# Optimization experiments

Measured on AMD Instinct MI355X. Metric: run time of the kernel, lower is better.

Reference implementation:

```python
import jax, jax.numpy as jnp
import numpy as np

N_NODES = 20000
N_EDGES = 400000
DIM = 128       # dim
NB = 16         # radial basis size
ZD = 16         # species encoding dim
N_SPECIES = 51
CUTOFF = 5.0
NLAYERS = 2
N_ONSITE = 3


def radial_basis(r):
    # 'gaussian_rinv': gaussians placed uniformly in inverse-distance space (HIP-NN style)
    rinv = 1.0 / r
    mus = jnp.linspace(1.0 / CUTOFF, 1.0, NB, dtype=r.dtype)
    sigma = mus[1] - mus[0]
    return jnp.exp(-0.5 * ((rinv[:, None] - mus[None, :]) / sigma) ** 2)  # [E, NB]


def setup_inputs() -> dict:
    key = jax.random.key(0)
    ks = jax.random.split(key, 16)
    species = jax.random.randint(ks[0], (N_NODES,), 1, N_SPECIES)
    edge_src = jax.random.randint(ks[1], (N_EDGES,), 0, N_NODES)
    edge_dst = jax.random.randint(ks[2], (N_EDGES,), 0, N_NODES)
    distances = jax.random.uniform(ks[3], (N_EDGES,), minval=0.8, maxval=CUTOFF)
    switch = jax.random.uniform(ks[4], (N_EDGES,))
    Z = jax.random.normal(ks[5], (N_SPECIES, ZD))  # species encoding table
    Ws0 = jax.random.normal(ks[6], (ZD, DIM)) / np.sqrt(ZD)
    bs0 = jnp.zeros((DIM,), jnp.float32)
    V0 = jax.random.normal(ks[7], (NB, ZD, DIM)) / np.sqrt(NB * ZD)
    Ws1 = jax.random.normal(ks[8], (DIM, DIM)) / np.sqrt(DIM)
    bs1 = jnp.zeros((DIM,), jnp.float32)
    V1 = jax.random.normal(ks[9], (NB, DIM, DIM)) / np.sqrt(NB * DIM)
    Won_a = jax.random.normal(ks[10], (NLAYERS, N_ONSITE, DIM, DIM)) / np.sqrt(DIM)
    bon_a = jnp.zeros((NLAYERS, N_ONSITE, DIM), jnp.float32)
    Won_b = jax.random.normal(ks[11], (NLAYERS, N_ONSITE, DIM, DIM)) / np.sqrt(DIM)
    bon_b = jnp.zeros((NLAYERS, N_ONSITE, DIM), jnp.float32)
    return dict(species=species, edge_src=edge_src, edge_dst=edge_dst,
                distances=distances, switch=switch, Z=Z,
                Ws0=Ws0, bs0=bs0, V0=V0, Ws1=Ws1, bs1=bs1, V1=V1,
                Won_a=Won_a, bon_a=bon_a, Won_b=Won_b, bon_b=bon_b)


def reference(species, edge_src, edge_dst, distances, switch, Z,
              Ws0, bs0, V0, Ws1, bs1, V1, Won_a, bon_a, Won_b, bon_b):
    zi = Z[species]                       # [N, ZD] species encoding
    s = radial_basis(distances)           # [E, NB] (identical basis each layer)
    sw = switch[:, None]                  # [E, 1]
    Ws, bs, Vs = (Ws0, Ws1), (bs0, bs1), (V0, V1)
    zis = []
    for layer in range(NLAYERS):
        zself = zi @ Ws[layer] + bs[layer]                        # [N, DIM]
        # mij = einsum('ej,ek,jkl->el', s, zi[edge_dst], V): per-edge outer then one GEMM
        zdst = zi[edge_dst]                                       # [E, k] gather
        outer = s[:, :, None] * zdst[:, None, :]                  # [E, NB, k]
        mij = outer.reshape(outer.shape[0], -1) @ Vs[layer].reshape(-1, DIM)  # [E, DIM]
        zi = jax.nn.silu(zself.at[edge_src].add(mij * sw))        # scatter-add
        for j in range(N_ONSITE):                                 # residual 2-layer MLPs
            h = jax.nn.silu(zi @ Won_a[layer, j] + bon_a[layer, j])
            zi = zi + h @ Won_b[layer, j] + bon_b[layer, j]
        zis.append(zi)
    # (embedding, embedding_layers)
    return zi, jnp.stack(zis, axis=1)
```

## Files before the change

kernel.cpp:

```cpp
#include <hip/hip_runtime.h>
#include <stdint.h>

#define NNODES 20000
#define NEDGES 400000
#define MTILES 1250
#define MT2    625
#define KS1 68

typedef __attribute__((ext_vector_type(8))) short short8;
typedef __attribute__((ext_vector_type(4))) float floatx4;

__device__ __forceinline__ float bf2f(uint16_t u){ return __uint_as_float(((uint32_t)u)<<16); }
__device__ __forceinline__ uint16_t f2bf(float f){
  uint32_t x = __float_as_uint(f);
  x += 0x7FFFu + ((x>>16)&1u);
  return (uint16_t)(x>>16);
}
__device__ __forceinline__ uint32_t packbf(float a, float b){
  return (uint32_t)f2bf(a) | ((uint32_t)f2bf(b)<<16);
}
__device__ __forceinline__ float siluf(float x){ return x/(1.0f+__expf(-x)); }
__device__ __forceinline__ float ldf(const void* p, int i, int md){
  return (md==1) ? bf2f(((const uint16_t*)p)[i]) : ((const float*)p)[i];
}

#define OFF_V0   0
#define N_V0     32768
#define OFF_WS1  32768
#define N_WS1    16384
#define OFF_BS1  49152
#define N_BS1    128
#define OFF_V1   49280
#define N_V1     262144
#define OFF_WA   311424
#define N_WA     98304
#define OFF_BA   409728
#define N_BA     768
#define OFF_WB   410496
#define N_WB     98304
#define OFF_BB   508800
#define N_BB     768
#define N_CONV   509568

__global__ void k_probe(const void* dist, int* mode){
  if(threadIdx.x != 0 || blockIdx.x != 0) return;
  const float* f = (const float*)dist;
  const uint16_t* h = (const uint16_t*)dist;
  int okf = 1, okb = 1;
  for(int i=0;i<256;i++){
    float a = f[i];       okf &= (a >= 0.7f) & (a <= 5.1f);
    float b = bf2f(h[i]); okb &= (b >= 0.7f) & (b <= 5.1f);
  }
  *mode = okb ? 1 : (okf ? 0 : 1);
}

__global__ __launch_bounds__(256) void k_conv(const void* s0,const void* s1,const void* s2,const void* s3,
                                              const void* s4,const void* s5,const void* s6,const void* s7,
                                              const int* __restrict__ modep, float* __restrict__ dst){
  int md = *modep;
  int i = blockIdx.x*256 + threadIdx.x;
  if(i >= N_CONV) return;
  const void* src; int t = i;
  if(t < N_V0){src=s0;}
  else if((t-=N_V0) < N_WS1){src=s1;}
  else if((t-=N_WS1) < N_BS1){src=s2;}
  else if((t-=N_BS1) < N_V1){src=s3;}
  else if((t-=N_V1) < N_WA){src=s4;}
  else if((t-=N_WA) < N_BA){src=s5;}
  else if((t-=N_BA) < N_WB){src=s6;}
  else {t-=N_WB; src=s7;}
  dst[i] = ldf(src, t, md);
}

__global__ __launch_bounds__(256) void k_hist(const int* __restrict__ src, int* __restrict__ cnt){
  int e = blockIdx.x*256 + threadIdx.x;
  if(e < NEDGES){
    int s = src[e];
    if((unsigned)s < NNODES) atomicAdd(&cnt[s], 1);
  }
}

__global__ __launch_bounds__(1024) void k_scan(int* cnt_cur, int* offs){
  __shared__ int wsum[16];
  int t = threadIdx.x;
  const int chunk = (NNODES + 1023)/1024;
  int lo = t*chunk, hi = lo+chunk;
  if(lo > NNODES) lo = NNODES;
  if(hi > NNODES) hi = NNODES;
  int s = 0;
  for(int i=lo;i<hi;i++) s += cnt_cur[i];
  int lane = t&63, wv = t>>6;
  int v = s;
  #pragma unroll
  for(int d=1; d<64; d<<=1){
    int u = __shfl_up(v, d);
    if(lane >= d) v += u;
  }
  if(lane==63) wsum[wv] = v;
  __syncthreads();
  if(t==0){
    int run = 0;
    #pragma unroll
    for(int i=0;i<16;i++){ int c = wsum[i]; wsum[i] = run; run += c; }
  }
  __syncthreads();
  int run = wsum[wv] + (v - s);
  for(int i=lo;i<hi;i++){
    int c = cnt_cur[i];
    offs[i] = run;
    cnt_cur[i] = run;
    run += c;
  }
  if(t==1023) offs[NNODES] = run;
}

__global__ __launch_bounds__(256) void k_fill(const int* __restrict__ src,
                                              const int* __restrict__ edst,
                                              const int* __restrict__ species,
                                              int* __restrict__ cur,
                                              int* __restrict__ dsts,
                                              int* __restrict__ sps,
                                              int* __restrict__ pos){
  int e = blockIdx.x*256 + threadIdx.x;
  if(e >= NEDGES) return;
  int s = src[e];
  if((unsigned)s >= NNODES) s = 0;
  int p = atomicAdd(&cur[s], 1);
  if((unsigned)p >= NEDGES) p = 0;
  pos[e] = p;
  int dn = edst[e];
  if((unsigned)dn >= NNODES) dn = 0;
  dsts[p] = dn;
  int sp = species[dn];
  if((unsigned)sp >= 51) sp = 0;
  sps[p] = sp;
}

__global__ __launch_bounds__(256) void k_G(const void* __restrict__ dist,
                                           const void* __restrict__ sw,
                                           const int* __restrict__ modep,
                                           const int* __restrict__ pos,
                                           uint16_t* __restrict__ gs){
  int e = blockIdx.x*256 + threadIdx.x;
  if(e >= NEDGES) return;
  int md = *modep;
  float r = ldf(dist, e, md);
  float w = ldf(sw, e, md);
  float rinv = 1.0f/r;
  const float sigma = 0.8f/15.0f;
  const float isig  = 15.0f/0.8f;
  uint32_t u[8];
  #pragma unroll
  for(int j=0;j<8;j++){
    float mu0 = 0.2f + sigma*(float)(2*j);
    float mu1 = 0.2f + sigma*(float)(2*j+1);
    float t0 = (rinv-mu0)*isig, t1 = (rinv-mu1)*isig;
    u[j] = packbf(w*__expf(-0.5f*t0*t0), w*__expf(-0.5f*t1*t1));
  }
  int p = pos[e];
  uint4* o = (uint4*)(gs + (size_t)p*16);
  o[0] = make_uint4(u[0],u[1],u[2],u[3]);
  o[1] = make_uint4(u[4],u[5],u[6],u[7]);
}

__global__ __launch_bounds__(128) void k_spec(const void* __restrict__ Z,
                                              const void* __restrict__ Ws0,
                                              const void* __restrict__ bs0,
                                              const int* __restrict__ modep,
                                              float* __restrict__ ZWs0,
                                              uint16_t* __restrict__ zfb){
  int s = blockIdx.x, d = threadIdx.x;
  int md = *modep;
  float zk[16];
  #pragma unroll
  for(int k=0;k<16;k++) zk[k] = ldf(Z, s*16+k, md);
  float a = ldf(bs0, d, md);
  #pragma unroll
  for(int k=0;k<16;k++) a = fmaf(zk[k], ldf(Ws0, k*128+d, md), a);
  ZWs0[s*128+d] = a;
  if(d < 16) zfb[s*16+d] = f2bf(zk[d]);
}

__global__ __launch_bounds__(256) void k_prepB(const float* __restrict__ W, int Ksteps,
                                               uint16_t* __restrict__ Bf){
  int idx = blockIdx.x*256 + threadIdx.x;
  int total = Ksteps*8*64;
  if(idx >= total) return;
  int l = idx & 63, nt = (idx>>6)&7, kk = idx>>9;
  int kbase = kk*32 + (l>>4)*8;
  int dim = nt*16 + (l&15);
  uint32_t u[4];
  #pragma unroll
  for(int t=0;t<4;t++){
    float f0 = W[(size_t)(kbase+2*t)*128 + dim];
    float f1 = W[(size_t)(kbase+2*t+1)*128 + dim];
    u[t] = packbf(f0,f1);
  }
  ((uint4*)Bf)[idx] = make_uint4(u[0],u[1],u[2],u[3]);
}

__global__ __launch_bounds__(256) void k_prepW(const float* __restrict__ conv,
                                               uint16_t* __restrict__ Wf){
  int idx = blockIdx.x*256 + threadIdx.x;
  if(idx >= 12*2048) return;
  int wi = idx>>11, r = idx&2047;
  int l = r & 63, nt = (r>>6)&7, kk = r>>9;
  const float* W = conv + ((wi<6) ? (OFF_WA + wi*16384) : (OFF_WB + (wi-6)*16384));
  int kbase = kk*32 + (l>>4)*8;
  int dim = nt*16 + (l&15);
  uint32_t u[4];
  #pragma unroll
  for(int t=0;t<4;t++){
    float f0 = W[(size_t)(kbase+2*t)*128 + dim];
    float f1 = W[(size_t)(kbase+2*t+1)*128 + dim];
    u[t] = packbf(f0,f1);
  }
  ((uint4*)Wf)[idx] = make_uint4(u[0],u[1],u[2],u[3]);
}

__global__ __launch_bounds__(256) void k_msg0f(const int* __restrict__ offs,
                                               const int* __restrict__ sps,
                                               const uint16_t* __restrict__ gs,
                                               const uint16_t* __restrict__ zfb,
                                               const uint16_t* __restrict__ Bf,
                                               const int* __restrict__ species,
                                               const float* __restrict__ ZWs0,
                                               float* __restrict__ zi){
  __shared__ uint16_t ldsA[8*64*8];
  int w = threadIdx.x>>6, l = threadIdx.x&63;
  int n0 = blockIdx.x*16;
  int col = l&15, quad = l>>4;
  for(int i=0;i<4;i++){
    int m = w*4 + i;
    int n = n0 + m;
    int beg = offs[n], end = offs[n+1];
    floatx4 acc0 = (floatx4){0.f,0.f,0.f,0.f};
    for(int p0=beg; p0<end; p0+=32){
      int sp[8];
      union { short8 s; uint16_t u[8]; } Bg, Az;
      #pragma unroll
      for(int j=0;j<8;j++){
        int p = p0 + quad*8 + j;
        int pc = p < end ? p : beg;
        sp[j] = sps[pc];
        uint16_t g = gs[(size_t)pc*16 + col];
        Bg.u[j] = (p < end) ? g : (uint16_t)0;
      }
      #pragma unroll
      for(int j=0;j<8;j++)
        Az.u[j] = zfb[sp[j]*16 + col];
      acc0 = __builtin_amdgcn_mfma_f32_16x16x32_bf16(Az.s, Bg.s, acc0, 0,0,0);
    }
    int K0 = col*16 + quad*4;
    int kk = K0>>5, qt = (K0>>3)&3, jt = K0&7;
    int slot = kk*64 + ((qt*16 + m) ^ (kk>>2));
    uint32_t lo = packbf(acc0[0], acc0[1]);
    uint32_t hi = packbf(acc0[2], acc0[3]);
    *(uint2*)(&ldsA[slot*8 + jt]) = make_uint2(lo, hi);
  }
  __syncthreads();
  floatx4 acc1 = (floatx4){0.f,0.f,0.f,0.f};
  floatx4 acc2 = (floatx4){0.f,0.f,0.f,0.f};
  const short8* Bp = (const short8*)Bf;
  int nt1 = w, nt2 = w+4;
  #pragma unroll
  for(int kk=0;kk<8;kk++){
    short8 a = *(const short8*)(&ldsA[(kk*64 + (l^(kk>>2)))*8]);
    short8 b1 = Bp[(size_t)(kk*8+nt1)*64 + l];
    short8 b2 = Bp[(size_t)(kk*8+nt2)*64 + l];
    acc1 = __builtin_amdgcn_mfma_f32_16x16x32_bf16(a, b1, acc1, 0,0,0);
    acc2 = __builtin_amdgcn_mfma_f32_16x16x32_bf16(a, b2, acc2, 0,0,0);
  }
  #pragma unroll
  for(int reg=0;reg<4;reg++){
    int node = n0 + quad*4 + reg;
    int sp = species[node];
    if((unsigned)sp >= 51) sp = 0;
    int d1 = nt1*16 + col, d2 = nt2*16 + col;
    zi[(size_t)node*128 + d1] = siluf(acc1[reg] + ZWs0[sp*128 + d1]);
    zi[(size_t)node*128 + d2] = siluf(acc2[reg] + ZWs0[sp*128 + d2]);
  }
}

__global__ __launch_bounds__(1024, 2) void k_msg1f(const int* __restrict__ offs,
                                               const int* __restrict__ dsts,
                                               const uint16_t* __restrict__ gs,
                                               const uint16_t* __restrict__ zib,
                                               const uint16_t* __restrict__ zib2,
                                               const uint16_t* __restrict__ Bf,
                                               const float* __restrict__ bias,
                                               float* __restrict__ zacc){
  __shared__ __align__(16) uint16_t ldsA[2*64*64*8];
  int w = threadIdx.x>>6, l = threadIdx.x&63;
  int n0 = blockIdx.x*32;
  int col = l&15, quad = l>>4;
  for(int i=0;i<2;i++){
    int m = w*2 + i;
    int n = n0 + m;
    int beg = offs[n], end = offs[n+1];
    floatx4 acc[8];
    #pragma unroll
    for(int t=0;t<8;t++) acc[t] = (floatx4){0.f,0.f,0.f,0.f};
    for(int p0=beg; p0<end; p0+=32){
      int dn[8];
      union { short8 s; uint16_t u[8]; } Bg;
      #pragma unroll
      for(int j=0;j<8;j++){
        int p = p0 + quad*8 + j;
        int pc = p < end ? p : beg;
        dn[j] = dsts[pc];
        uint16_t g = gs[(size_t)pc*16 + col];
        Bg.u[j] = (p < end) ? g : (uint16_t)0;
      }
      uint4 row[8];
      #pragma unroll
      for(int j=0;j<8;j++)
        row[j] = *(const uint4*)(zib2 + (size_t)dn[j]*128 + col*8);
      #pragma unroll
      for(int mt=0;mt<8;mt++){
        union { short8 s; uint32_t u32[4]; } Az;
        #pragma unroll
        for(int cp=0;cp<4;cp++){
          uint32_t a = ((const uint32_t*)&row[2*cp])[mt>>1];
          uint32_t b = ((const uint32_t*)&row[2*cp+1])[mt>>1];
          Az.u32[cp] = __builtin_amdgcn_perm(b, a, (mt&1) ? 0x07060302u : 0x05040100u);
        }
        acc[mt] = __builtin_amdgcn_mfma_f32_16x16x32_bf16(Az.s, Bg.s, acc[mt], 0,0,0);
      }
    }
    uint16_t* tile = ldsA + (size_t)(m>>4)*32768;
    int mloc = m & 15;
    #pragma unroll
    for(int mt=0;mt<8;mt++){
      int K0 = col*128 + mt*16 + quad*4;
      int kk = K0>>5, qt = (K0>>3)&3, jt = K0&7;
      int slot = kk*64 + ((qt*16 + mloc) ^ (kk>>2));
      uint32_t lo = packbf(acc[mt][0], acc[mt][1]);
      uint32_t hi = packbf(acc[mt][2], acc[mt][3]);
      *(uint2*)(&tile[slot*8 + jt]) = make_uint2(lo, hi);
    }
  }
  __syncthreads();
  int nt1 = w & 7, half = w >> 3;
  floatx4 accA = (floatx4){0.f,0.f,0.f,0.f};
  floatx4 accB = (floatx4){0.f,0.f,0.f,0.f};
  const short8* Bp = (const short8*)Bf;
  int kb = half*32, ke = kb + 32;
  #pragma unroll 8
  for(int kk=kb;kk<ke;kk++){
    int ai = (kk*64 + (l^(kk>>2)))*8;
    short8 a0 = *(const short8*)(&ldsA[ai]);
    short8 a1 = *(const short8*)(&ldsA[32768 + ai]);
    short8 b1 = Bp[(size_t)(kk*8+nt1)*64 + l];
    accA = __builtin_amdgcn_mfma_f32_16x16x32_bf16(a0, b1, accA, 0,0,0);
    accB = __builtin_amdgcn_mfma_f32_16x16x32_bf16(a1, b1, accB, 0,0,0);
  }
  #pragma unroll
  for(int t=0;t<2;t++){
    int kk = 64 + half*2 + t;
    uint4 za0 = *(const uint4*)(zib + (size_t)(n0+col)*128 + (kk-64)*32 + quad*8);
    uint4 za1 = *(const uint4*)(zib + (size_t)(n0+16+col)*128 + (kk-64)*32 + quad*8);
    union { short8 s; uint4 u; } A0, A1; A0.u = za0; A1.u = za1;
    short8 b1 = Bp[(size_t)(kk*8+nt1)*64 + l];
    accA = __builtin_amdgcn_mfma_f32_16x16x32_bf16(A0.s, b1, accA, 0,0,0);
    accB = __builtin_amdgcn_mfma_f32_16x16x32_bf16(A1.s, b1, accB, 0,0,0);
  }
  __syncthreads();
  float* red = (float*)ldsA;
  if(half==1){
    *(floatx4*)(&red[(nt1*64 + l)*4])     = accA;
    *(floatx4*)(&red[((8+nt1)*64 + l)*4]) = accB;
  }
  __syncthreads();
  if(half==0){
    floatx4 o0 = *(const floatx4*)(&red[(nt1*64 + l)*4]);
    floatx4 o1 = *(const floatx4*)(&red[((8+nt1)*64 + l)*4]);
    int d1 = nt1*16 + col;
    float bv = bias[d1];
    #pragma unroll
    for(int reg=0;reg<4;reg++){
      int nodeA = n0 + quad*4 + reg;
      int nodeB = n0 + 16 + quad*4 + reg;
      zacc[(size_t)nodeA*128 + d1] = siluf(accA[reg] + o0[reg] + bv);
      zacc[(size_t)nodeB*128 + d1] = siluf(accB[reg] + o1[reg] + bv);
    }
  }
}

__global__ __launch_bounds__(256) void k_onsite(float* __restrict__ zi,
                                                const uint16_t* __restrict__ Waf,
                                                const float* __restrict__ ba,
                                                const uint16_t* __restrict__ Wbf,
                                                const float* __restrict__ bb,
                                                void* __restrict__ outb,
                                                long off1, int st1,
                                                long off2, int st2,
                                                const int* __restrict__ modep,
                                                uint16_t* __restrict__ zib,
                                                uint16_t* __restrict__ zib2){
  __shared__ float zb[16*132];
  __shared__ float hb[16*132];
  int w = threadIdx.x>>6, l = threadIdx.x&63;
  int mtile = blockIdx.x;
  int n0 = mtile*16;
  int md = *modep;
  #pragma unroll
  for(int i=0;i<2;i++){
    int flat = (i*256 + threadIdx.x)*4;
    int node = flat>>7, k = flat&127;
    *(float4*)(zb + node*132 + k) = *(const float4*)(zi + (size_t)(n0+node)*128 + k);
  }
  __syncthreads();
  int m = l&15, q = l>>4;
  for(int j=0;j<3;j++){
    const short8* Ba = (const short8*)Waf + (size_t)j*2048 + l;
    floatx4 acc[2];
    acc[0] = (floatx4){0.f,0.f,0.f,0.f};
    acc[1] = (floatx4){0.f,0.f,0.f,0.f};
    #pragma unroll
    for(int kk=0;kk<4;kk++){
      const float* zp = zb + m*132 + kk*32 + q*8;
      float4 a0 = *(const float4*)zp, a1 = *(const float4*)(zp+4);
      union { short8 s; uint32_t u[4]; } A;
      A.u[0]=packbf(a0.x,a0.y); A.u[1]=packbf(a0.z,a0.w);
      A.u[2]=packbf(a1.x,a1.y); A.u[3]=packbf(a1.z,a1.w);
      #pragma unroll
      for(int t=0;t<2;t++){
        short8 bfr = Ba[(size_t)(kk*8 + w*2+t)*64];
        acc[t] = __builtin_amdgcn_mfma_f32_16x16x32_bf16(A.s, bfr, acc[t], 0,0,0);
      }
    }
    #pragma unroll
    for(int t=0;t<2;t++){
      int dim = (w*2+t)*16 + m;
      float bv = ba[j*128+dim];
      #pragma unroll
      for(int reg=0;reg<4;reg++)
        hb[(q*4+reg)*132 + dim] = siluf(acc[t][reg] + bv);
    }
    __syncthreads();
    const short8* Bb = (const short8*)Wbf + (size_t)j*2048 + l;
    floatx4 acc2[2];
    acc2[0] = (floatx4){0.f,0.f,0.f,0.f};
    acc2[1] = (floatx4){0.f,0.f,0.f,0.f};
    #pragma unroll
    for(int kk=0;kk<4;kk++){
      const float* hp = hb + m*132 + kk*32 + q*8;
      float4 a0 = *(const float4*)hp, a1 = *(const float4*)(hp+4);
      union { short8 s; uint32_t u[4]; } A;
      A.u[0]=packbf(a0.x,a0.y); A.u[1]=packbf(a0.z,a0.w);
      A.u[2]=packbf(a1.x,a1.y); A.u[3]=packbf(a1.z,a1.w);
      #pragma unroll
      for(int t=0;t<2;t++){
        short8 bfr = Bb[(size_t)(kk*8 + w*2+t)*64];
        acc2[t] = __builtin_amdgcn_mfma_f32_16x16x32_bf16(A.s, bfr, acc2[t], 0,0,0);
      }
    }
    #pragma unroll
    for(int t=0;t<2;t++){
      int dim = (w*2+t)*16 + m;
      float bv = bb[j*128+dim];
      #pragma unroll
      for(int reg=0;reg<4;reg++){
        int idx = (q*4+reg)*132 + dim;
        zb[idx] = zb[idx] + acc2[t][reg] + bv;
      }
    }
    __syncthreads();
  }
  #pragma unroll
  for(int i=0;i<2;i++){
    int flat = (i*256 + threadIdx.x)*4;
    int node = flat>>7, k = flat&127;
    float4 v = *(float4*)(zb + node*132 + k);
    int n = n0 + node;
    *(float4*)(zi + (size_t)n*128 + k) = v;
    uint2 pv = make_uint2(packbf(v.x,v.y), packbf(v.z,v.w));
    if(zib) *(uint2*)(zib + (size_t)n*128 + k) = pv;
    if(md==1){
      uint16_t* ob = (uint16_t*)outb;
      *(uint2*)(ob + off1 + (long)n*st1 + k) = pv;
      if(off2 >= 0) *(uint2*)(ob + off2 + (long)n*st2 + k) = pv;
    } else {
      float* ob = (float*)outb;
      *(float4*)(ob + off1 + (long)n*st1 + k) = v;
      if(off2 >= 0) *(float4*)(ob + off2 + (long)n*st2 + k) = v;
    }
  }
  if(zib2){
    int node2 = threadIdx.x>>4, c = threadIdx.x&15;
    float vv[8];
    #pragma unroll
    for(int mt=0;mt<8;mt++) vv[mt] = zb[node2*132 + mt*16 + c];
    uint4 o = make_uint4(packbf(vv[0],vv[1]), packbf(vv[2],vv[3]),
                         packbf(vv[4],vv[5]), packbf(vv[6],vv[7]));
    *(uint4*)(zib2 + (size_t)(n0+node2)*128 + c*8) = o;
  }
}

extern "C" void kernel_launch(void* const* d_in, const int* in_sizes, int n_in,
                              void* d_out, int out_size, void* d_ws, size_t ws_size,
                              hipStream_t stream){
  const int* species = (const int*)d_in[0];
  const int* esrc    = (const int*)d_in[1];
  const int* edst    = (const int*)d_in[2];
  const void* dist   = d_in[3];
  const void* swit   = d_in[4];
  const void* Z      = d_in[5];
  const void* Ws0    = d_in[6];
  const void* bs0    = d_in[7];
  const void* V0     = d_in[8];
  const void* Ws1    = d_in[9];
  const void* bs1    = d_in[10];
  const void* V1     = d_in[11];
  const void* Wa     = d_in[12];
  const void* ba     = d_in[13];
  const void* Wb     = d_in[14];
  const void* bb     = d_in[15];

  char* ws = (char*)d_ws;
  size_t off = 0;
  auto alloc = [&](size_t bytes)->void*{ void* p = ws + off; off = (off + bytes + 255) & ~(size_t)255; return p; };
  int*      offs = (int*)     alloc((size_t)(NNODES+1)*4);
  int*      cur  = (int*)     alloc((size_t)NNODES*4);
  int*      pos  = (int*)     alloc((size_t)NEDGES*4);
  int*      dsts = (int*)     alloc((size_t)NEDGES*4);
  int*      sps  = (int*)     alloc((size_t)NEDGES*4);
  uint16_t* gs   = (uint16_t*)alloc((size_t)NEDGES*16*2);
  float*    zi   = (float*)   alloc((size_t)NNODES*128*4);
  float*    zacc = (float*)   alloc((size_t)NNODES*128*4);
  uint16_t* zib  = (uint16_t*)alloc((size_t)NNODES*128*2);
  uint16_t* zib2 = (uint16_t*)alloc((size_t)NNODES*128*2);
  float*    ZWs0 = (float*)   alloc((size_t)51*128*4);
  uint16_t* zfb  = (uint16_t*)alloc((size_t)51*16*2);
  float*    conv = (float*)   alloc((size_t)N_CONV*4);
  uint16_t* Bf0  = (uint16_t*)alloc((size_t)8*8*64*8*2);
  uint16_t* Bf1  = (uint16_t*)alloc((size_t)KS1*8*64*8*2);
  uint16_t* Wfr  = (uint16_t*)alloc((size_t)12*16384*2);
  int*      mode = (int*)     alloc(256);

  const int EB = (NEDGES+255)/256;
  hipMemsetAsync(cur, 0, NNODES*4, stream);
  k_probe<<<1,64,0,stream>>>(dist, mode);
  k_conv <<<(N_CONV+255)/256,256,0,stream>>>(V0, Ws1, bs1, V1, Wa, ba, Wb, bb, mode, conv);
  k_hist <<<EB,256,0,stream>>>(esrc, cur);
  k_scan <<<1,1024,0,stream>>>(cur, offs);
  k_fill <<<EB,256,0,stream>>>(esrc, edst, species, cur, dsts, sps, pos);
  k_G    <<<EB,256,0,stream>>>(dist, swit, mode, pos, gs);
  k_spec <<<51,128,0,stream>>>(Z, Ws0, bs0, mode, ZWs0, zfb);
  k_prepB<<<(8*8*64+255)/256,256,0,stream>>>(conv+OFF_V0, 8,  Bf0);
  k_prepB<<<(64*8*64+255)/256,256,0,stream>>>(conv+OFF_V1, 64, Bf1);
  k_prepB<<<(4*8*64+255)/256,256,0,stream>>>(conv+OFF_WS1, 4, Bf1 + (size_t)64*8*64*8);
  k_prepW<<<(12*2048+255)/256,256,0,stream>>>(conv, Wfr);

  const long ZIS = (long)NNODES*128;
  uint16_t* WaF0 = Wfr;
  uint16_t* WaF1 = Wfr + (size_t)3*16384;
  uint16_t* WbF0 = Wfr + (size_t)6*16384;
  uint16_t* WbF1 = Wfr + (size_t)9*16384;

  k_msg0f<<<MTILES,256,0,stream>>>(offs, sps, gs, zfb, Bf0, species, ZWs0, zi);
  k_onsite<<<MTILES,256,0,stream>>>(zi, WaF0, conv+OFF_BA, WbF0, conv+OFF_BB,
                                    d_out, ZIS, 256, (long)-1, 0, mode, zib, zib2);

  k_msg1f<<<MT2,1024,0,stream>>>(offs, dsts, gs, zib, zib2, Bf1, conv+OFF_BS1, zacc);
  k_onsite<<<MTILES,256,0,stream>>>(zacc, WaF1, conv+OFF_BA+384, WbF1, conv+OFF_BB+384,
                                    d_out, ZIS+128, 256, (long)0, 128, mode,
                                    (uint16_t*)nullptr, (uint16_t*)nullptr);
}
```

Before: 295.4 us.

## Fuse onsite MLPs into message kernels and merge fill with radial basis

Merges the edge fill kernel with the radial-basis kernel so the pos array round-trip and one launch disappear. Fuses the three residual onsite MLP blocks into each layer's message-passing kernel, keeping the node tile in shared memory instead of writing fp32 zi/zacc to global memory and reading it back. This removes two launches and about 20 MB of intermediate traffic per layer. In exchange it raises shared memory and register pressure in the fused kernels, and the layer-1 kernel now splits its 16 waves into two 8-wave groups of 16 nodes each.

```diff
diff --git a/kernel.cpp b/kernel.cpp
--- a/kernel.cpp
+++ b/kernel.cpp
@@ -114,36 +114,29 @@
   if(t==1023) offs[NNODES] = run;
 }
 
-__global__ __launch_bounds__(256) void k_fill(const int* __restrict__ src,
-                                              const int* __restrict__ edst,
-                                              const int* __restrict__ species,
-                                              int* __restrict__ cur,
-                                              int* __restrict__ dsts,
-                                              int* __restrict__ sps,
-                                              int* __restrict__ pos){
+__global__ __launch_bounds__(256) void k_fillG(const int* __restrict__ src,
+                                               const int* __restrict__ edst,
+                                               const int* __restrict__ species,
+                                               int* __restrict__ cur,
+                                               const void* __restrict__ dist,
+                                               const void* __restrict__ sw,
+                                               const int* __restrict__ modep,
+                                               int* __restrict__ dsts,
+                                               int* __restrict__ sps,
+                                               uint16_t* __restrict__ gs){
   int e = blockIdx.x*256 + threadIdx.x;
   if(e >= NEDGES) return;
+  int md = *modep;
   int s = src[e];
   if((unsigned)s >= NNODES) s = 0;
   int p = atomicAdd(&cur[s], 1);
   if((unsigned)p >= NEDGES) p = 0;
-  pos[e] = p;
   int dn = edst[e];
   if((unsigned)dn >= NNODES) dn = 0;
   dsts[p] = dn;
   int sp = species[dn];
   if((unsigned)sp >= 51) sp = 0;
   sps[p] = sp;
-}
-
-__global__ __launch_bounds__(256) void k_G(const void* __restrict__ dist,
-                                           const void* __restrict__ sw,
-                                           const int* __restrict__ modep,
-                                           const int* __restrict__ pos,
-                                           uint16_t* __restrict__ gs){
-  int e = blockIdx.x*256 + threadIdx.x;
-  if(e >= NEDGES) return;
-  int md = *modep;
   float r = ldf(dist, e, md);
   float w = ldf(sw, e, md);
   float rinv = 1.0f/r;
@@ -157,7 +150,6 @@
     float t0 = (rinv-mu0)*isig, t1 = (rinv-mu1)*isig;
     u[j] = packbf(w*__expf(-0.5f*t0*t0), w*__expf(-0.5f*t1*t1));
   }
-  int p = pos[e];
   uint4* o = (uint4*)(gs + (size_t)p*16);
   o[0] = make_uint4(u[0],u[1],u[2],u[3]);
   o[1] = make_uint4(u[4],u[5],u[6],u[7]);
@@ -218,15 +210,24 @@
   ((uint4*)Wf)[idx] = make_uint4(u[0],u[1],u[2],u[3]);
 }
 
-__global__ __launch_bounds__(256) void k_msg0f(const int* __restrict__ offs,
-                                               const int* __restrict__ sps,
-                                               const uint16_t* __restrict__ gs,
-                                               const uint16_t* __restrict__ zfb,
-                                               const uint16_t* __restrict__ Bf,
-                                               const int* __restrict__ species,
-                                               const float* __restrict__ ZWs0,
-                                               float* __restrict__ zi){
+__global__ __launch_bounds__(256) void k_l0(const int* __restrict__ offs,
+                                            const int* __restrict__ sps,
+                                            const uint16_t* __restrict__ gs,
+                                            const uint16_t* __restrict__ zfb,
+                                            const uint16_t* __restrict__ Bf,
+                                            const int* __restrict__ species,
+                                            const float* __restrict__ ZWs0,
+                                            const uint16_t* __restrict__ Waf,
+                                            const float* __restrict__ ba,
+                                            const uint16_t* __restrict__ Wbf,
+                                            const float* __restrict__ bb,
+                                            void* __restrict__ outb,
+                                            const int* __restrict__ modep,
+                                            uint16_t* __restrict__ zib,
+                                            uint16_t* __restrict__ zib2){
   __shared__ uint16_t ldsA[8*64*8];
+  __shared__ float zb[16*132];
+  __shared__ float hb[16*132];
   int w = threadIdx.x>>6, l = threadIdx.x&63;
   int n0 = blockIdx.x*16;
   int col = l&15, quad = l>>4;
@@ -277,19 +278,110 @@
     int sp = species[node];
     if((unsigned)sp >= 51) sp = 0;
     int d1 = nt1*16 + col, d2 = nt2*16 + col;
-    zi[(size_t)node*128 + d1] = siluf(acc1[reg] + ZWs0[sp*128 + d1]);
-    zi[(size_t)node*128 + d2] = siluf(acc2[reg] + ZWs0[sp*128 + d2]);
-  }
-}
-
-__global__ __launch_bounds__(1024, 2) void k_msg1f(const int* __restrict__ offs,
+    int row = quad*4 + reg;
+    zb[row*132 + d1] = siluf(acc1[reg] + ZWs0[sp*128 + d1]);
+    zb[row*132 + d2] = siluf(acc2[reg] + ZWs0[sp*128 + d2]);
+  }
+  __syncthreads();
+  int m = col, q = quad;
+  for(int j=0;j<3;j++){
+    const short8* Ba = (const short8*)Waf + (size_t)j*2048 + l;
+    floatx4 acc[2];
+    acc[0] = (floatx4){0.f,0.f,0.f,0.f};
+    acc[1] = (floatx4){0.f,0.f,0.f,0.f};
+    #pragma unroll
+    for(int kk=0;kk<4;kk++){
+      const float* zp = zb + m*132 + kk*32 + q*8;
+      float4 a0 = *(const float4*)zp, a1 = *(const float4*)(zp+4);
+      union { short8 s; uint32_t u[4]; } A;
+      A.u[0]=packbf(a0.x,a0.y); A.u[1]=packbf(a0.z,a0.w);
+      A.u[2]=packbf(a1.x,a1.y); A.u[3]=packbf(a1.z,a1.w);
+      #pragma unroll
+      for(int t=0;t<2;t++){
+        short8 bfr = Ba[(size_t)(kk*8 + w*2+t)*64];
+        acc[t] = __builtin_amdgcn_mfma_f32_16x16x32_bf16(A.s, bfr, acc[t], 0,0,0);
+      }
+    }
+    #pragma unroll
+    for(int t=0;t<2;t++){
+      int dim = (w*2+t)*16 + m;
+      float bv = ba[j*128+dim];
+      #pragma unroll
+      for(int reg=0;reg<4;reg++)
+        hb[(q*4+reg)*132 + dim] = siluf(acc[t][reg] + bv);
+    }
+    __syncthreads();
+    const short8* Bb = (const short8*)Wbf + (size_t)j*2048 + l;
+    floatx4 acc2o[2];
+    acc2o[0] = (floatx4){0.f,0.f,0.f,0.f};
+    acc2o[1] = (floatx4){0.f,0.f,0.f,0.f};
+    #pragma unroll
+    for(int kk=0;kk<4;kk++){
+      const float* hp = hb + m*132 + kk*32 + q*8;
+      float4 a0 = *(const float4*)hp, a1 = *(const float4*)(hp+4);
+      union { short8 s; uint32_t u[4]; } A;
+      A.u[0]=packbf(a0.x,a0.y); A.u[1]=packbf(a0.z,a0.w);
+      A.u[2]=packbf(a1.x,a1.y); A.u[3]=packbf(a1.z,a1.w);
+      #pragma unroll
+      for(int t=0;t<2;t++){
+        short8 bfr = Bb[(size_t)(kk*8 + w*2+t)*64];
+        acc2o[t] = __builtin_amdgcn_mfma_f32_16x16x32_bf16(A.s, bfr, acc2o[t], 0,0,0);
+      }
+    }
+    #pragma unroll
+    for(int t=0;t<2;t++){
+      int dim = (w*2+t)*16 + m;
+      float bv = bb[j*128+dim];
+      #pragma unroll
+      for(int reg=0;reg<4;reg++){
+        int idx = (q*4+reg)*132 + dim;
+        zb[idx] = zb[idx] + acc2o[t][reg] + bv;
+      }
+    }
+    __syncthreads();
+  }
+  int md = *modep;
+  const long ZIS = (long)NNODES*128;
+  #pragma unroll
+  for(int i=0;i<2;i++){
+    int flat = (i*256 + threadIdx.x)*4;
+    int node = flat>>7, k = flat&127;
+    float4 v = *(float4*)(zb + node*132 + k);
+    int n = n0 + node;
+    uint2 pv = make_uint2(packbf(v.x,v.y), packbf(v.z,v.w));
+    *(uint2*)(zib + (size_t)n*128 + k) = pv;
+    if(md==1){
+      uint16_t* ob = (uint16_t*)outb;
+      *(uint2*)(ob + ZIS + (long)n*256 + k) = pv;
+    } else {
+      float* ob = (float*)outb;
+      *(float4*)(ob + ZIS + (long)n*256 + k) = v;
+    }
+  }
+  {
+    int node2 = threadIdx.x>>4, c = threadIdx.x&15;
+    float vv[8];
+    #pragma unroll
+    for(int mt=0;mt<8;mt++) vv[mt] = zb[node2*132 + mt*16 + c];
+    uint4 o = make_uint4(packbf(vv[0],vv[1]), packbf(vv[2],vv[3]),
+                         packbf(vv[4],vv[5]), packbf(vv[6],vv[7]));
+    *(uint4*)(zib2 + (size_t)(n0+node2)*128 + c*8) = o;
+  }
+}
+
+__global__ __launch_bounds__(1024, 2) void k_l1(const int* __restrict__ offs,
                                                const int* __restrict__ dsts,
                                                const uint16_t* __restrict__ gs,
                                                const uint16_t* __restrict__ zib,
                                                const uint16_t* __restrict__ zib2,
                                                const uint16_t* __restrict__ Bf,
                                                const float* __restrict__ bias,
-                                               float* __restrict__ zacc){
+                                               const uint16_t* __restrict__ Waf,
+                                               const float* __restrict__ ba,
+                                               const uint16_t* __restrict__ Wbf,
+                                               const float* __restrict__ bb,
+                                               void* __restrict__ outb,
+                                               const int* __restrict__ modep){
   __shared__ __align__(16) uint16_t ldsA[2*64*64*8];
   int w = threadIdx.x>>6, l = threadIdx.x&63;
   int n0 = blockIdx.x*32;
@@ -367,6 +459,10 @@
   }
   __syncthreads();
   float* red = (float*)ldsA;
+  float* zbA = (float*)((char*)ldsA + 16384);
+  float* zbB = zbA + 16*132;
+  float* hbA = zbB + 16*132;
+  float* hbB = hbA + 16*132;
   if(half==1){
     *(floatx4*)(&red[(nt1*64 + l)*4])     = accA;
     *(floatx4*)(&red[((8+nt1)*64 + l)*4]) = accB;
@@ -379,44 +475,19 @@
     float bv = bias[d1];
     #pragma unroll
     for(int reg=0;reg<4;reg++){
-      int nodeA = n0 + quad*4 + reg;
-      int nodeB = n0 + 16 + quad*4 + reg;
-      zacc[(size_t)nodeA*128 + d1] = siluf(accA[reg] + o0[reg] + bv);
-      zacc[(size_t)nodeB*128 + d1] = siluf(accB[reg] + o1[reg] + bv);
-    }
-  }
-}
-
-__global__ __launch_bounds__(256) void k_onsite(float* __restrict__ zi,
-                                                const uint16_t* __restrict__ Waf,
-                                                const float* __restrict__ ba,
-                                                const uint16_t* __restrict__ Wbf,
-                                                const float* __restrict__ bb,
-                                                void* __restrict__ outb,
-                                                long off1, int st1,
-                                                long off2, int st2,
-                                                const int* __restrict__ modep,
-                                                uint16_t* __restrict__ zib,
-                                                uint16_t* __restrict__ zib2){
-  __shared__ float zb[16*132];
-  __shared__ float hb[16*132];
-  int w = threadIdx.x>>6, l = threadIdx.x&63;
-  int mtile = blockIdx.x;
-  int n0 = mtile*16;
-  int md = *modep;
-  #pragma unroll
-  for(int i=0;i<2;i++){
-    int flat = (i*256 + threadIdx.x)*4;
-    int node = flat>>7, k = flat&127;
-    *(float4*)(zb + node*132 + k) = *(const float4*)(zi + (size_t)(n0+node)*128 + k);
-  }
-  __syncthreads();
-  int m = l&15, q = l>>4;
+      int row = quad*4 + reg;
+      zbA[row*132 + d1] = siluf(accA[reg] + o0[reg] + bv);
+      zbB[row*132 + d1] = siluf(accB[reg] + o1[reg] + bv);
+    }
+  }
+  __syncthreads();
+  int grp = w>>3, wl = w&7;
+  float* zb = grp ? zbB : zbA;
+  float* hb = grp ? hbB : hbA;
+  int m = col, q = quad;
   for(int j=0;j<3;j++){
     const short8* Ba = (const short8*)Waf + (size_t)j*2048 + l;
-    floatx4 acc[2];
-    acc[0] = (floatx4){0.f,0.f,0.f,0.f};
-    acc[1] = (floatx4){0.f,0.f,0.f,0.f};
+    floatx4 acc = (floatx4){0.f,0.f,0.f,0.f};
     #pragma unroll
     for(int kk=0;kk<4;kk++){
       const float* zp = zb + m*132 + kk*32 + q*8;
@@ -424,25 +495,19 @@
       union { short8 s; uint32_t u[4]; } A;
       A.u[0]=packbf(a0.x,a0.y); A.u[1]=packbf(a0.z,a0.w);
       A.u[2]=packbf(a1.x,a1.y); A.u[3]=packbf(a1.z,a1.w);
-      #pragma unroll
-      for(int t=0;t<2;t++){
-        short8 bfr = Ba[(size_t)(kk*8 + w*2+t)*64];
-        acc[t] = __builtin_amdgcn_mfma_f32_16x16x32_bf16(A.s, bfr, acc[t], 0,0,0);
-      }
-    }
-    #pragma unroll
-    for(int t=0;t<2;t++){
-      int dim = (w*2+t)*16 + m;
+      short8 bfr = Ba[(size_t)(kk*8 + wl)*64];
+      acc = __builtin_amdgcn_mfma_f32_16x16x32_bf16(A.s, bfr, acc, 0,0,0);
+    }
+    {
+      int dim = wl*16 + m;
       float bv = ba[j*128+dim];
       #pragma unroll
       for(int reg=0;reg<4;reg++)
-        hb[(q*4+reg)*132 + dim] = siluf(acc[t][reg] + bv);
+        hb[(q*4+reg)*132 + dim] = siluf(acc[reg] + bv);
     }
     __syncthreads();
     const short8* Bb = (const short8*)Wbf + (size_t)j*2048 + l;
-    floatx4 acc2[2];
-    acc2[0] = (floatx4){0.f,0.f,0.f,0.f};
-    acc2[1] = (floatx4){0.f,0.f,0.f,0.f};
+    floatx4 acc2 = (floatx4){0.f,0.f,0.f,0.f};
     #pragma unroll
     for(int kk=0;kk<4;kk++){
       const float* hp = hb + m*132 + kk*32 + q*8;
@@ -450,51 +515,37 @@
       union { short8 s; uint32_t u[4]; } A;
       A.u[0]=packbf(a0.x,a0.y); A.u[1]=packbf(a0.z,a0.w);
       A.u[2]=packbf(a1.x,a1.y); A.u[3]=packbf(a1.z,a1.w);
-      #pragma unroll
-      for(int t=0;t<2;t++){
-        short8 bfr = Bb[(size_t)(kk*8 + w*2+t)*64];
-        acc2[t] = __builtin_amdgcn_mfma_f32_16x16x32_bf16(A.s, bfr, acc2[t], 0,0,0);
-      }
-    }
-    #pragma unroll
-    for(int t=0;t<2;t++){
-      int dim = (w*2+t)*16 + m;
+      short8 bfr = Bb[(size_t)(kk*8 + wl)*64];
+      acc2 = __builtin_amdgcn_mfma_f32_16x16x32_bf16(A.s, bfr, acc2, 0,0,0);
+    }
+    {
+      int dim = wl*16 + m;
       float bv = bb[j*128+dim];
       #pragma unroll
       for(int reg=0;reg<4;reg++){
         int idx = (q*4+reg)*132 + dim;
-        zb[idx] = zb[idx] + acc2[t][reg] + bv;
+        zb[idx] = zb[idx] + acc2[reg] + bv;
       }
     }
     __syncthreads();
   }
-  #pragma unroll
-  for(int i=0;i<2;i++){
-    int flat = (i*256 + threadIdx.x)*4;
-    int node = flat>>7, k = flat&127;
+  {
+    int md = *modep;
+    const long ZIS = (long)NNODES*128;
+    int tig = wl*64 + l;
+    int flat = tig*4, node = flat>>7, k = flat&127;
     float4 v = *(float4*)(zb + node*132 + k);
-    int n = n0 + node;
-    *(float4*)(zi + (size_t)n*128 + k) = v;
-    uint2 pv = make_uint2(packbf(v.x,v.y), packbf(v.z,v.w));
-    if(zib) *(uint2*)(zib + (size_t)n*128 + k) = pv;
+    int n = n0 + grp*16 + node;
     if(md==1){
+      uint2 pv = make_uint2(packbf(v.x,v.y), packbf(v.z,v.w));
       uint16_t* ob = (uint16_t*)outb;
-      *(uint2*)(ob + off1 + (long)n*st1 + k) = pv;
-      if(off2 >= 0) *(uint2*)(ob + off2 + (long)n*st2 + k) = pv;
+      *(uint2*)(ob + ZIS + 128 + (long)n*256 + k) = pv;
+      *(uint2*)(ob + (long)n*128 + k) = pv;
     } else {
       float* ob = (float*)outb;
-      *(float4*)(ob + off1 + (long)n*st1 + k) = v;
-      if(off2 >= 0) *(float4*)(ob + off2 + (long)n*st2 + k) = v;
-    }
-  }
-  if(zib2){
-    int node2 = threadIdx.x>>4, c = threadIdx.x&15;
-    float vv[8];
-    #pragma unroll
-    for(int mt=0;mt<8;mt++) vv[mt] = zb[node2*132 + mt*16 + c];
-    uint4 o = make_uint4(packbf(vv[0],vv[1]), packbf(vv[2],vv[3]),
-                         packbf(vv[4],vv[5]), packbf(vv[6],vv[7]));
-    *(uint4*)(zib2 + (size_t)(n0+node2)*128 + c*8) = o;
+      *(float4*)(ob + ZIS + 128 + (long)n*256 + k) = v;
+      *(float4*)(ob + (long)n*128 + k) = v;
+    }
   }
 }
 
@@ -523,12 +574,9 @@
   auto alloc = [&](size_t bytes)->void*{ void* p = ws + off; off = (off + bytes + 255) & ~(size_t)255; return p; };
   int*      offs = (int*)     alloc((size_t)(NNODES+1)*4);
   int*      cur  = (int*)     alloc((size_t)NNODES*4);
-  int*      pos  = (int*)     alloc((size_t)NEDGES*4);
   int*      dsts = (int*)     alloc((size_t)NEDGES*4);
   int*      sps  = (int*)     alloc((size_t)NEDGES*4);
   uint16_t* gs   = (uint16_t*)alloc((size_t)NEDGES*16*2);
-  float*    zi   = (float*)   alloc((size_t)NNODES*128*4);
-  float*    zacc = (float*)   alloc((size_t)NNODES*128*4);
   uint16_t* zib  = (uint16_t*)alloc((size_t)NNODES*128*2);
   uint16_t* zib2 = (uint16_t*)alloc((size_t)NNODES*128*2);
   float*    ZWs0 = (float*)   alloc((size_t)51*128*4);
@@ -545,26 +593,23 @@
   k_conv <<<(N_CONV+255)/256,256,0,stream>>>(V0, Ws1, bs1, V1, Wa, ba, Wb, bb, mode, conv);
   k_hist <<<EB,256,0,stream>>>(esrc, cur);
   k_scan <<<1,1024,0,stream>>>(cur, offs);
-  k_fill <<<EB,256,0,stream>>>(esrc, edst, species, cur, dsts, sps, pos);
-  k_G    <<<EB,256,0,stream>>>(dist, swit, mode, pos, gs);
+  k_fillG<<<EB,256,0,stream>>>(esrc, edst, species, cur, dist, swit, mode, dsts, sps, gs);
   k_spec <<<51,128,0,stream>>>(Z, Ws0, bs0, mode, ZWs0, zfb);
   k_prepB<<<(8*8*64+255)/256,256,0,stream>>>(conv+OFF_V0, 8,  Bf0);
   k_prepB<<<(64*8*64+255)/256,256,0,stream>>>(conv+OFF_V1, 64, Bf1);
   k_prepB<<<(4*8*64+255)/256,256,0,stream>>>(conv+OFF_WS1, 4, Bf1 + (size_t)64*8*64*8);
   k_prepW<<<(12*2048+255)/256,256,0,stream>>>(conv, Wfr);
 
-  const long ZIS = (long)NNODES*128;
   uint16_t* WaF0 = Wfr;
   uint16_t* WaF1 = Wfr + (size_t)3*16384;
   uint16_t* WbF0 = Wfr + (size_t)6*16384;
   uint16_t* WbF1 = Wfr + (size_t)9*16384;
 
-  k_msg0f<<<MTILES,256,0,stream>>>(offs, sps, gs, zfb, Bf0, species, ZWs0, zi);
-  k_onsite<<<MTILES,256,0,stream>>>(zi, WaF0, conv+OFF_BA, WbF0, conv+OFF_BB,
-                                    d_out, ZIS, 256, (long)-1, 0, mode, zib, zib2);
-
-  k_msg1f<<<MT2,1024,0,stream>>>(offs, dsts, gs, zib, zib2, Bf1, conv+OFF_BS1, zacc);
-  k_onsite<<<MTILES,256,0,stream>>>(zacc, WaF1, conv+OFF_BA+384, WbF1, conv+OFF_BB+384,
-                                    d_out, ZIS+128, 256, (long)0, 128, mode,
-                                    (uint16_t*)nullptr, (uint16_t*)nullptr);
-}
+  k_l0<<<MTILES,256,0,stream>>>(offs, sps, gs, zfb, Bf0, species, ZWs0,
+                                WaF0, conv+OFF_BA, WbF0, conv+OFF_BB,
+                                d_out, mode, zib, zib2);
+
+  k_l1<<<MT2,1024,0,stream>>>(offs, dsts, gs, zib, zib2, Bf1, conv+OFF_BS1,
+                              WaF1, conv+OFF_BA+384, WbF1, conv+OFF_BB+384,
+                              d_out, mode);
+}
```

Measured after the change: 297.1 us. No clear change (+0.6%).
